# Kernel optimization log

Measured on AMD Instinct MI355X. Metric: run time of the kernel, lower is better.

## Reference

```python
import jax, jax.numpy as jnp
import numpy as np

N = 64       # number of nodes (features)
K = 512      # sequence length
WIN = 5
KS = 5       # conv kernel size
EMBED = 64   # embed_dim


def setup_inputs() -> dict:
    key = jax.random.key(0)
    ks = jax.random.split(key, 8)
    x = jax.random.normal(ks[0], (N, K), dtype=jnp.float32)
    # fully connected graph without self loops (remove_self_loops is then a no-op)
    src, dst = np.nonzero(~np.eye(N, dtype=bool))
    edge_index = jnp.asarray(np.stack([src, dst]), dtype=jnp.int32)  # [2, E]
    conv_w = jax.random.normal(ks[1], (1, 1, KS), dtype=jnp.float32) * 0.3
    conv_b = jnp.zeros((1,), jnp.float32)
    s = 1.0 / np.sqrt(WIN)
    lin_l_w = jax.random.uniform(ks[2], (EMBED, WIN), jnp.float32, -s, s)
    lin_l_b = jax.random.uniform(ks[3], (EMBED,), jnp.float32, -s, s)
    lin_r_w = jax.random.uniform(ks[4], (EMBED, WIN), jnp.float32, -s, s)
    lin_r_b = jax.random.uniform(ks[5], (EMBED,), jnp.float32, -s, s)
    glorot = np.sqrt(6.0 / (1 + EMBED))
    att = jax.random.uniform(ks[6], (1, EMBED), jnp.float32, -glorot, glorot)
    return dict(x=x, edge_index=edge_index, conv_w=conv_w, conv_b=conv_b,
                lin_l_w=lin_l_w, lin_l_b=lin_l_b, lin_r_w=lin_r_w,
                lin_r_b=lin_r_b, att=att)


def reference(x, edge_index, conv_w, conv_b, lin_l_w, lin_l_b, lin_r_w, lin_r_b, att):
    n_temp = K - WIN + 1
    # Conv1d(1,1,KS, padding='same') + sigmoid
    h = jax.lax.conv_general_dilated(x[:, None, :], conv_w, window_strides=(1,),
                                     padding='SAME',
                                     dimension_numbers=('NCH', 'OIH', 'NCH'))
    h = jax.nn.sigmoid(h[:, 0, :] + conv_b)                      # [N, K]
    widx = jnp.arange(n_temp)[:, None] + jnp.arange(WIN)[None, :]
    xw = h[:, widx].reshape(-1, WIN)
    # temporal edge index: node idx -> idx*n_temp + t
    t = jnp.arange(n_temp)[None, :]
    l = (edge_index[0][:, None] * n_temp + t).reshape(-1)        # [E*n_temp]
    r = (edge_index[1][:, None] * n_temp + t).reshape(-1)
    x_l = xw @ lin_l_w.T + lin_l_b                               # [N*n_temp, EMBED]
    x_r = xw @ lin_r_w.T + lin_r_b
    e = jax.nn.leaky_relu(x_l[l] + x_r[r], negative_slope=0.2)   # [E*n_temp, EMBED]
    alpha = (e * att).sum(-1)                                    # [E*n_temp]
    # segment softmax grouped by source temporal node l
    S = N * n_temp
    m = jax.ops.segment_max(alpha, l, num_segments=S)
    a = jnp.exp(alpha - m[l])
    denom = jax.ops.segment_sum(a, l, num_segments=S)
    alpha = a / (denom[l] + 1e-16)
    return alpha.reshape(-1, n_temp)                             # [E, n_temp]
```

## Files before the change

kernel.cpp:

```cpp
#include <hip/hip_runtime.h>

#define NNODE 64
#define KLEN  512
#define WIN   5
#define NT    508
#define EMB   64
#define NDST  63

typedef float v2f __attribute__((ext_vector_type(2)));

#define H_OFF  0
#define XL_OFF ((size_t)NNODE * KLEN)

__device__ __forceinline__ int xr_idx(int n, int d) {
    return n * EMB + ((((d >> 2) ^ (n & 7)) << 2) | (d & 3));
}

__device__ __forceinline__ float sigmoid_f(float a) {
    return __builtin_amdgcn_rcpf(1.f + __expf(-a));
}

__global__ __launch_bounds__(256) void conv_h(
    const float* __restrict__ x,
    const float* __restrict__ conv_w,
    const float* __restrict__ conv_b,
    float* __restrict__ ws)
{
    const int n = blockIdx.x >> 1;
    const int k = ((blockIdx.x & 1) << 8) + threadIdx.x;
    float acc = conv_b[0];
    #pragma unroll
    for (int j = 0; j < WIN; ++j) {
        const int kk = k + j - 2;
        const float xv = (kk >= 0 && kk < KLEN) ? x[n * KLEN + kk] : 0.f;
        acc = fmaf(conv_w[j], xv, acc);
    }
    ws[H_OFF + n * KLEN + k] = sigmoid_f(acc);
}

__global__ __launch_bounds__(256) void build_xl(
    const float* __restrict__ lin_l_w,
    const float* __restrict__ lin_l_b,
    float* __restrict__ ws)
{
    const int bx  = blockIdx.x;
    const int t   = (bx & 7) * 64 + ((bx >> 3) >> 2);
    if (t >= NT) return;
    const int nc  = (bx >> 3) & 3;
    const int tid  = threadIdx.x;
    const int lane = tid & 63;
    const int wave = tid >> 6;

    float lw[WIN];
    #pragma unroll
    for (int w = 0; w < WIN; ++w) lw[w] = lin_l_w[lane * WIN + w];
    const float lb = lin_l_b[lane];

    const float* h_g = ws + H_OFF;
    float* xl_ws = ws + XL_OFF + (size_t)t * NNODE * EMB;
    #pragma unroll
    for (int i = 0; i < 4; ++i) {
        const int n = nc * 16 + wave * 4 + i;
        const float* hn = h_g + n * KLEN + t;
        float xl = lb;
        #pragma unroll
        for (int w = 0; w < WIN; ++w)
            xl = fmaf(lw[w], hn[w], xl);
        xl_ws[n * EMB + lane] = xl;
    }
}

__global__ __launch_bounds__(256) void attn_main(
    const float* __restrict__ lin_r_w,
    const float* __restrict__ lin_r_b,
    const float* __restrict__ att,
    const float* __restrict__ ws,
    float* __restrict__ out)
{
    const int bx = blockIdx.x;
    const int t  = (bx & 7) * 64 + (bx >> 3);
    if (t >= NT) return;
    const int sg   = blockIdx.y;
    const int tid  = threadIdx.x;
    const int lane = tid & 63;
    const int wave = tid >> 6;

    __shared__ float xr_s[NNODE * EMB];

    {
        float rw[WIN];
        #pragma unroll
        for (int w = 0; w < WIN; ++w) rw[w] = lin_r_w[lane * WIN + w];
        const float rb = lin_r_b[lane];
        const float* h_g = ws + H_OFF;
        #pragma unroll
        for (int k = 0; k < 16; ++k) {
            const int n = wave + 4 * k;
            const float* hn = h_g + n * KLEN + t;
            float xr = rb;
            #pragma unroll
            for (int w = 0; w < WIN; ++w)
                xr = fmaf(rw[w], hn[w], xr);
            xr_s[xr_idx(n, lane)] = xr;
        }
    }

    const int wu = __builtin_amdgcn_readfirstlane(wave);
    const int s0 = sg * 16 + wu * 4;
    const float* xl_g = ws + XL_OFF + (size_t)t * NNODE * EMB + (size_t)s0 * EMB;

    __syncthreads();

    v2f acc2[4], accB2;
    #pragma unroll
    for (int p = 0; p < 4; ++p) acc2[p] = (v2f)(0.f);
    accB2 = (v2f)(0.f);

    float4 xlc[4], xln[4];
    #pragma unroll
    for (int p = 0; p < 4; ++p)
        xlc[p] = *(const float4*)(xl_g + p * EMB);

    #pragma unroll
    for (int d0 = 0; d0 < EMB; d0 += 4) {
        if (d0 + 4 < EMB) {
            #pragma unroll
            for (int p = 0; p < 4; ++p)
                xln[p] = *(const float4*)(xl_g + p * EMB + d0 + 4);
        }
        const float4 xr4 = *(const float4*)&xr_s[xr_idx(lane, d0)];
        const v2f xr01 = {xr4.x, xr4.y};
        const v2f xr23 = {xr4.z, xr4.w};
        const v2f a01  = *(const v2f*)(att + d0);
        const v2f a23  = *(const v2f*)(att + d0 + 2);
        accB2 = __builtin_elementwise_fma(a01, xr01, accB2);
        accB2 = __builtin_elementwise_fma(a23, xr23, accB2);
        #pragma unroll
        for (int p = 0; p < 4; ++p) {
            const v2f xl01 = {xlc[p].x, xlc[p].y};
            const v2f xl23 = {xlc[p].z, xlc[p].w};
            v2f z01 = xl01 + xr01;
            v2f z23 = xl23 + xr23;
            v2f m01 = __builtin_elementwise_max(z01, -z01);
            v2f m23 = __builtin_elementwise_max(z23, -z23);
            acc2[p] = __builtin_elementwise_fma(a01, m01, acc2[p]);
            acc2[p] = __builtin_elementwise_fma(a23, m23, acc2[p]);
        }
        #pragma unroll
        for (int p = 0; p < 4; ++p) xlc[p] = xln[p];
    }
    const float accB = accB2.x + accB2.y;

    float ex[4];
    #pragma unroll
    for (int p = 0; p < 4; ++p) {
        const int s = s0 + p;
        const float alpha = fmaf(0.4f, acc2[p].x + acc2[p].y, 0.6f * accB);
        ex[p] = (lane == s) ? 0.f : __expf(alpha);
    }
    float sum[4];
    #pragma unroll
    for (int p = 0; p < 4; ++p) sum[p] = ex[p];
    #pragma unroll
    for (int off = 32; off; off >>= 1) {
        #pragma unroll
        for (int p = 0; p < 4; ++p) sum[p] += __shfl_xor(sum[p], off);
    }
    #pragma unroll
    for (int p = 0; p < 4; ++p) {
        const int s = s0 + p;
        const float res = ex[p] * __builtin_amdgcn_rcpf(sum[p] + 1e-16f);
        if (lane != s) {
            const int j = lane - (lane > s ? 1 : 0);
            out[(size_t)(s * NDST + j) * NT + t] = res;
        }
    }
}

extern "C" void kernel_launch(void* const* d_in, const int* in_sizes, int n_in,
                              void* d_out, int out_size, void* d_ws, size_t ws_size,
                              hipStream_t stream)
{
    const float* x       = (const float*)d_in[0];
    const float* conv_w  = (const float*)d_in[2];
    const float* conv_b  = (const float*)d_in[3];
    const float* lin_l_w = (const float*)d_in[4];
    const float* lin_l_b = (const float*)d_in[5];
    const float* lin_r_w = (const float*)d_in[6];
    const float* lin_r_b = (const float*)d_in[7];
    const float* att     = (const float*)d_in[8];
    float* out = (float*)d_out;
    float* ws  = (float*)d_ws;

    conv_h<<<dim3(128), 256, 0, stream>>>(x, conv_w, conv_b, ws);
    build_xl<<<dim3(2048), 256, 0, stream>>>(lin_l_w, lin_l_b, ws);
    attn_main<<<dim3(512, 4), 256, 0, stream>>>(lin_r_w, lin_r_b, att, ws, out);
}
```

Measured before the change: 31.57 us.

## Fuse x_l projection into attention kernel, keep x_l tile in LDS

Removes the separate build_xl kernel and its global x_l workspace (508*64*64 floats written then read back). Each attention block now computes its 16 source rows of x_l directly from h and stores them in shared memory before the barrier. The packed v2f arithmetic and global prefetch are replaced with scalar fabsf/fma on LDS reads. This drops one launch and a large round trip through global memory, at the cost of some extra compute per block and more LDS use.

Result: faster. 30.23 us (-4.2%).

```diff
diff --git a/kernel.cpp b/kernel.cpp
--- a/kernel.cpp
+++ b/kernel.cpp
@@ -7,10 +7,7 @@
 #define EMB   64
 #define NDST  63
 
-typedef float v2f __attribute__((ext_vector_type(2)));
-
-#define H_OFF  0
-#define XL_OFF ((size_t)NNODE * KLEN)
+#define H_OFF 0
 
 __device__ __forceinline__ int xr_idx(int n, int d) {
     return n * EMB + ((((d >> 2) ^ (n & 7)) << 2) | (d & 3));
@@ -38,39 +35,9 @@
     ws[H_OFF + n * KLEN + k] = sigmoid_f(acc);
 }
 
-__global__ __launch_bounds__(256) void build_xl(
+__global__ __launch_bounds__(256) void attn_all(
     const float* __restrict__ lin_l_w,
     const float* __restrict__ lin_l_b,
-    float* __restrict__ ws)
-{
-    const int bx  = blockIdx.x;
-    const int t   = (bx & 7) * 64 + ((bx >> 3) >> 2);
-    if (t >= NT) return;
-    const int nc  = (bx >> 3) & 3;
-    const int tid  = threadIdx.x;
-    const int lane = tid & 63;
-    const int wave = tid >> 6;
-
-    float lw[WIN];
-    #pragma unroll
-    for (int w = 0; w < WIN; ++w) lw[w] = lin_l_w[lane * WIN + w];
-    const float lb = lin_l_b[lane];
-
-    const float* h_g = ws + H_OFF;
-    float* xl_ws = ws + XL_OFF + (size_t)t * NNODE * EMB;
-    #pragma unroll
-    for (int i = 0; i < 4; ++i) {
-        const int n = nc * 16 + wave * 4 + i;
-        const float* hn = h_g + n * KLEN + t;
-        float xl = lb;
-        #pragma unroll
-        for (int w = 0; w < WIN; ++w)
-            xl = fmaf(lw[w], hn[w], xl);
-        xl_ws[n * EMB + lane] = xl;
-    }
-}
-
-__global__ __launch_bounds__(256) void attn_main(
     const float* __restrict__ lin_r_w,
     const float* __restrict__ lin_r_b,
     const float* __restrict__ att,
@@ -84,18 +51,25 @@
     const int tid  = threadIdx.x;
     const int lane = tid & 63;
     const int wave = tid >> 6;
+    const int wu   = __builtin_amdgcn_readfirstlane(wave);
 
     __shared__ float xr_s[NNODE * EMB];
+    __shared__ float xl_s[16][EMB];
 
     {
-        float rw[WIN];
+        float rw[WIN], lw[WIN];
         #pragma unroll
-        for (int w = 0; w < WIN; ++w) rw[w] = lin_r_w[lane * WIN + w];
+        for (int w = 0; w < WIN; ++w) {
+            rw[w] = lin_r_w[lane * WIN + w];
+            lw[w] = lin_l_w[lane * WIN + w];
+        }
         const float rb = lin_r_b[lane];
+        const float lb = lin_l_b[lane];
         const float* h_g = ws + H_OFF;
+
         #pragma unroll
         for (int k = 0; k < 16; ++k) {
-            const int n = wave + 4 * k;
+            const int n = wu + 4 * k;
             const float* hn = h_g + n * KLEN + t;
             float xr = rb;
             #pragma unroll
@@ -103,59 +77,50 @@
                 xr = fmaf(rw[w], hn[w], xr);
             xr_s[xr_idx(n, lane)] = xr;
         }
+        #pragma unroll
+        for (int i = 0; i < 4; ++i) {
+            const int sl = wu * 4 + i;
+            const int n  = sg * 16 + sl;
+            const float* hn = h_g + n * KLEN + t;
+            float xl = lb;
+            #pragma unroll
+            for (int w = 0; w < WIN; ++w)
+                xl = fmaf(lw[w], hn[w], xl);
+            xl_s[sl][lane] = xl;
+        }
+    }
+    __syncthreads();
+
+    float accm[4] = {0.f, 0.f, 0.f, 0.f};
+    float accB = 0.f;
+    #pragma unroll
+    for (int d0 = 0; d0 < EMB; d0 += 4) {
+        const float4 xr4 = *(const float4*)&xr_s[xr_idx(lane, d0)];
+        const float a0 = att[d0 + 0];
+        const float a1 = att[d0 + 1];
+        const float a2 = att[d0 + 2];
+        const float a3 = att[d0 + 3];
+        accB = fmaf(a0, xr4.x, accB);
+        accB = fmaf(a1, xr4.y, accB);
+        accB = fmaf(a2, xr4.z, accB);
+        accB = fmaf(a3, xr4.w, accB);
+        #pragma unroll
+        for (int p = 0; p < 4; ++p) {
+            const float4 xl4 = *(const float4*)&xl_s[wave * 4 + p][d0];
+            float z;
+            z = xl4.x + xr4.x; accm[p] = fmaf(a0, fabsf(z), accm[p]);
+            z = xl4.y + xr4.y; accm[p] = fmaf(a1, fabsf(z), accm[p]);
+            z = xl4.z + xr4.z; accm[p] = fmaf(a2, fabsf(z), accm[p]);
+            z = xl4.w + xr4.w; accm[p] = fmaf(a3, fabsf(z), accm[p]);
+        }
     }
 
-    const int wu = __builtin_amdgcn_readfirstlane(wave);
     const int s0 = sg * 16 + wu * 4;
-    const float* xl_g = ws + XL_OFF + (size_t)t * NNODE * EMB + (size_t)s0 * EMB;
-
-    __syncthreads();
-
-    v2f acc2[4], accB2;
-    #pragma unroll
-    for (int p = 0; p < 4; ++p) acc2[p] = (v2f)(0.f);
-    accB2 = (v2f)(0.f);
-
-    float4 xlc[4], xln[4];
-    #pragma unroll
-    for (int p = 0; p < 4; ++p)
-        xlc[p] = *(const float4*)(xl_g + p * EMB);
-
-    #pragma unroll
-    for (int d0 = 0; d0 < EMB; d0 += 4) {
-        if (d0 + 4 < EMB) {
-            #pragma unroll
-            for (int p = 0; p < 4; ++p)
-                xln[p] = *(const float4*)(xl_g + p * EMB + d0 + 4);
-        }
-        const float4 xr4 = *(const float4*)&xr_s[xr_idx(lane, d0)];
-        const v2f xr01 = {xr4.x, xr4.y};
-        const v2f xr23 = {xr4.z, xr4.w};
-        const v2f a01  = *(const v2f*)(att + d0);
-        const v2f a23  = *(const v2f*)(att + d0 + 2);
-        accB2 = __builtin_elementwise_fma(a01, xr01, accB2);
-        accB2 = __builtin_elementwise_fma(a23, xr23, accB2);
-        #pragma unroll
-        for (int p = 0; p < 4; ++p) {
-            const v2f xl01 = {xlc[p].x, xlc[p].y};
-            const v2f xl23 = {xlc[p].z, xlc[p].w};
-            v2f z01 = xl01 + xr01;
-            v2f z23 = xl23 + xr23;
-            v2f m01 = __builtin_elementwise_max(z01, -z01);
-            v2f m23 = __builtin_elementwise_max(z23, -z23);
-            acc2[p] = __builtin_elementwise_fma(a01, m01, acc2[p]);
-            acc2[p] = __builtin_elementwise_fma(a23, m23, acc2[p]);
-        }
-        #pragma unroll
-        for (int p = 0; p < 4; ++p) xlc[p] = xln[p];
-    }
-    const float accB = accB2.x + accB2.y;
-
     float ex[4];
     #pragma unroll
     for (int p = 0; p < 4; ++p) {
         const int s = s0 + p;
-        const float alpha = fmaf(0.4f, acc2[p].x + acc2[p].y, 0.6f * accB);
+        const float alpha = fmaf(0.4f, accm[p], 0.6f * accB);
         ex[p] = (lane == s) ? 0.f : __expf(alpha);
     }
     float sum[4];
@@ -193,6 +158,6 @@
     float* ws  = (float*)d_ws;
 
     conv_h<<<dim3(128), 256, 0, stream>>>(x, conv_w, conv_b, ws);
-    build_xl<<<dim3(2048), 256, 0, stream>>>(lin_l_w, lin_l_b, ws);
-    attn_main<<<dim3(512, 4), 256, 0, stream>>>(lin_r_w, lin_r_b, att, ws, out);
+    attn_all<<<dim3(512, 4), 256, 0, stream>>>(lin_l_w, lin_l_b,
+        lin_r_w, lin_r_b, att, ws, out);
 }
```
